# Optimization experiments

Hardware: AMD Instinct MI355X
Metric: run time of the kernel (lower is better)

Reference implementation:

```python
import jax, jax.numpy as jnp
import numpy as np
from jax import lax

EPS = 1e-5

def _silu(x):
    return x * jax.nn.sigmoid(x)

def _mamba_seq(x, ln_w, ln_b, in_w, conv_w, conv_b, xp_w, dt_w, dt_b, A_log, Dp, out_w):
    # x: [B, L, dim] token sequence
    di = conv_w.shape[0]          # d_inner
    ds = A_log.shape[1]           # d_state
    dtr = dt_w.shape[1]           # dt_rank
    kw = conv_w.shape[2]          # d_conv
    # LayerNorm
    mu = jnp.mean(x, axis=-1, keepdims=True)
    var = jnp.mean((x - mu) ** 2, axis=-1, keepdims=True)
    xn = (x - mu) * lax.rsqrt(var + EPS) * ln_w + ln_b
    # in_proj -> (x, z)
    xz = xn @ in_w.T                       # [B,L,2*di]
    xs, z = xz[..., :di], xz[..., di:]
    # causal depthwise conv1d over L
    xc = lax.conv_general_dilated(xs.transpose(0, 2, 1), conv_w, (1,),
                                  [(kw - 1, 0)], feature_group_count=di,
                                  dimension_numbers=('NCH', 'OIH', 'NCH'))
    xc = _silu(xc + conv_b[None, :, None]).transpose(0, 2, 1)   # [B,L,di]
    # x_proj -> dt, B, C
    dbc = xc @ xp_w.T                      # [B,L,dtr+2*ds]
    dt = jax.nn.softplus(dbc[..., :dtr] @ dt_w.T + dt_b)        # [B,L,di]
    Bm = dbc[..., dtr:dtr + ds]            # [B,L,ds]
    Cm = dbc[..., dtr + ds:]               # [B,L,ds]
    A = -jnp.exp(A_log)                    # [di,ds]
    dA = jnp.exp(dt[..., None] * A)        # [B,L,di,ds]
    dBu = (dt * xc)[..., None] * Bm[:, :, None, :]              # [B,L,di,ds]
    # selective scan: h_t = dA_t * h_{t-1} + dBu_t (parallel associative scan)
    def comb(e1, e2):
        a1, b1 = e1
        a2, b2 = e2
        return a1 * a2, a2 * b1 + b2
    _, h = lax.associative_scan(comb, (dA, dBu), axis=1)
    y = jnp.einsum('blds,bls->bld', h, Cm) + xc * Dp
    return (y * _silu(z)) @ out_w.T

def _mamba_block(x5, *p):
    # x5: [B,C,D,H,W] -> flatten spatial dims to tokens
    B, C = x5.shape[:2]
    xf = x5.reshape(B, C, -1).transpose(0, 2, 1)   # [B,L,C]
    y = _mamba_seq(xf, *p)
    return y.transpose(0, 2, 1).reshape(x5.shape)

def _conv3d(x, w, b):
    return lax.conv_general_dilated(x, w, (1, 1, 1), [(1, 1)] * 3,
                                    dimension_numbers=('NCDHW', 'OIDHW', 'NCDHW')) \
           + b[None, :, None, None, None]

def _bn3d(x, g, b):
    # BatchNorm3d in training mode: batch statistics over (B,D,H,W)
    m = jnp.mean(x, axis=(0, 2, 3, 4), keepdims=True)
    v = jnp.mean((x - m) ** 2, axis=(0, 2, 3, 4), keepdims=True)
    return (x - m) * lax.rsqrt(v + EPS) * g.reshape(1, -1, 1, 1, 1) + b.reshape(1, -1, 1, 1, 1)

def _mamba_params(key, dim, d_state=16, d_conv=4, expand=2):
    di = expand * dim
    dtr = max(1, -(-dim // 16))
    ks = jax.random.split(key, 5)
    return {
        'ln_w': jnp.ones((dim,), jnp.float32),
        'ln_b': jnp.zeros((dim,), jnp.float32),
        'in_w': jax.random.normal(ks[0], (2 * di, dim), jnp.float32) * (dim ** -0.5),
        'conv_w': jax.random.normal(ks[1], (di, 1, d_conv), jnp.float32) * 0.3,
        'conv_b': jnp.zeros((di,), jnp.float32),
        'xp_w': jax.random.normal(ks[2], (dtr + 2 * d_state, di), jnp.float32) * (di ** -0.5),
        'dt_w': jax.random.normal(ks[3], (di, dtr), jnp.float32) * (dtr ** -0.5),
        'dt_b': jnp.log(jnp.expm1(jnp.full((di,), 0.01, jnp.float32))),
        'A_log': jnp.log(jnp.tile(jnp.arange(1, d_state + 1, dtype=jnp.float32)[None, :], (di, 1))),
        'D': jnp.ones((di,), jnp.float32),
        'out_w': jax.random.normal(ks[4], (dim, di), jnp.float32) * (di ** -0.5),
    }

def setup_inputs() -> dict:
    key = jax.random.key(0)
    k = jax.random.split(key, 8)
    inp = {
        'l': jax.random.normal(k[0], (1, 16, 16, 48, 48), jnp.float32),
        's': jax.random.normal(k[1], (1, 16, 16, 48, 48), jnp.float32),
    }
    for name, p in _mamba_params(k[2], 32).items():
        inp['m1_' + name] = p
    for name, p in _mamba_params(k[3], 16).items():
        inp['m2_' + name] = p
    inp['c1_w'] = jax.random.normal(k[4], (16, 32, 3, 3, 3), jnp.float32) * ((32 * 27) ** -0.5)
    inp['c1_b'] = jnp.zeros((16,), jnp.float32)
    inp['bn1_g'] = jnp.ones((16,), jnp.float32)
    inp['bn1_b'] = jnp.zeros((16,), jnp.float32)
    inp['c2_w'] = jax.random.normal(k[5], (16, 16, 3, 3, 3), jnp.float32) * ((16 * 27) ** -0.5)
    inp['c2_b'] = jnp.zeros((16,), jnp.float32)
    inp['bn2_g'] = jnp.ones((16,), jnp.float32)
    inp['bn2_b'] = jnp.zeros((16,), jnp.float32)
    return inp

def reference(l, s,
              m1_ln_w, m1_ln_b, m1_in_w, m1_conv_w, m1_conv_b, m1_xp_w, m1_dt_w, m1_dt_b, m1_A_log, m1_D, m1_out_w,
              m2_ln_w, m2_ln_b, m2_in_w, m2_conv_w, m2_conv_b, m2_xp_w, m2_dt_w, m2_dt_b, m2_A_log, m2_D, m2_out_w,
              c1_w, c1_b, bn1_g, bn1_b, c2_w, c2_b, bn2_g, bn2_b):
    x = jnp.concatenate([l, s], axis=1)                         # [B,32,D,H,W]
    x = _mamba_block(x, m1_ln_w, m1_ln_b, m1_in_w, m1_conv_w, m1_conv_b,
                     m1_xp_w, m1_dt_w, m1_dt_b, m1_A_log, m1_D, m1_out_w) + x
    x = _bn3d(_conv3d(x, c1_w, c1_b), bn1_g, bn1_b)             # [B,16,D,H,W]
    x = _mamba_block(x, m2_ln_w, m2_ln_b, m2_in_w, m2_conv_w, m2_conv_b,
                     m2_xp_w, m2_dt_w, m2_dt_b, m2_A_log, m2_D, m2_out_w) + x
    x = _bn3d(_conv3d(x, c2_w, c2_b), bn2_g, bn2_b)
    return x
```

## Files before the change

### kernel.cpp

```cpp
#include <hip/hip_runtime.h>
#include <math.h>

#define L_TOT 36864
#define BN_EPS 1e-5f
#define PCH 45000

typedef __attribute__((ext_vector_type(8))) short bf16x8;
typedef __attribute__((ext_vector_type(4))) float f32x4;

__device__ __forceinline__ float fsigmoid(float x){ return 1.f/(1.f+__expf(-x)); }
__device__ __forceinline__ float fsoftplus(float x){
  float e = __expf(x);
  return (x>20.f)? x : __logf(1.f+e);
}
__device__ __forceinline__ unsigned short f2bf(float x){
  union { float f; unsigned u; } cv; cv.f = x;
  unsigned r = (cv.u + 0x7FFFu + ((cv.u>>16)&1u)) >> 16;
  return (unsigned short)r;
}
__host__ __device__ constexpr int off3c(int r){
  return (r>=27) ? 0 : ((r/9)-1)*2500 + (((r%9)/3)-1)*50 + ((r%3)-1);
}

__global__ void k_setup(const float* __restrict__ w1, unsigned short* __restrict__ wA1,
                        const float* __restrict__ w2, unsigned short* __restrict__ wA2,
                        float* __restrict__ stats, float* __restrict__ bfz) {
  int b = blockIdx.x, tid = threadIdx.x;
  int idx = b*256 + tid;
  if (idx < 16*PCH) bfz[idx] = 0.f;
  if (b < 4){
    int k = b*256 + tid;
    if (k < 864){
      int ic = k & 31, r = k >> 5;
      for (int m=0;m<16;m++){
        float v = (r < 27) ? w1[m*32*27 + ic*27 + r] : 0.f;
        wA1[(((k>>3)*16) + m)*8 + (k&7)] = f2bf(v);
      }
    }
  } else if (b < 6){
    int k = (b-4)*256 + tid;
    if (k < 448){
      int ic = k & 15, r = k >> 4;
      for (int m=0;m<16;m++){
        float v = (r < 27) ? w2[m*16*27 + ic*27 + r] : 0.f;
        wA2[(((k>>3)*16) + m)*8 + (k&7)] = f2bf(v);
      }
    }
  } else if (b == 6){
    if (tid < 64) stats[tid] = 0.f;
  }
}

template<int DIM, int DI, int DTR, bool DOBN>
__global__ __launch_bounds__(256) void k_front(
    const float* __restrict__ x0, const float* __restrict__ x1,
    const float* __restrict__ bstats, const float* __restrict__ bg, const float* __restrict__ bbp,
    const float* __restrict__ lnw, const float* __restrict__ lnb,
    const float* __restrict__ inw,
    const float* __restrict__ cw, const float* __restrict__ cb,
    const float* __restrict__ xpw,
    const float* __restrict__ dtw, const float* __restrict__ dtb,
    const float* __restrict__ Alog,
    float* __restrict__ xcg, float* __restrict__ zg,
    float* __restrict__ dtpg, float* __restrict__ Bg, float* __restrict__ Cg,
    float* __restrict__ aggA, float* __restrict__ aggB)
{
  constexpr int TCH  = 48;
  constexpr int ROWS = DTR + 32;
  constexpr int NSH  = 256/DI;
  constexpr int SPB  = 16/NSH;
  constexpr int O_SX  = 0;
  constexpr int O_SXS = O_SX + DIM*64;
  constexpr int O_SDT = O_SXS;
  constexpr int O_SXC = O_SXS + DI*64;
  constexpr int O_SB  = O_SXC + DI*49;
  constexpr int O_SC  = O_SB + 16*49;
  constexpr int O_DTP = O_SC + 16*49;
  constexpr int SMEM  = O_DTP + DTR*48 + 64;
  __shared__ float sm[SMEM];

  const int tid   = threadIdx.x;
  const int chunk = blockIdx.x;
  const int t0    = chunk*TCH;

  for (int idx = tid; idx < DIM*64; idx += 256){
    int c = idx >> 6, i = idx & 63;
    int t = t0 - 3 + i;
    float v = 0.f;
    if (i < 51 && t >= 0){
      if constexpr (DOBN){
        float raw = x0[c*L_TOT + t];
        float bm = bstats[2*c]*(1.f/L_TOT);
        float bv = bstats[2*c+1]*(1.f/L_TOT) - bm*bm;
        v = (raw - bm)*rsqrtf(bv+BN_EPS)*bg[c] + bbp[c];
      } else {
        v = (c < 16) ? x0[c*L_TOT + t] : x1[(c-16)*L_TOT + t];
      }
    }
    sm[O_SX + idx] = v;
  }
  __syncthreads();

  if (tid < 64){
    float s = 0.f, s2 = 0.f;
#pragma unroll
    for (int c = 0; c < DIM; c++){
      float v = sm[O_SX + c*64 + tid];
      s += v; s2 += v*v;
    }
    float m  = s*(1.f/DIM);
    float var = s2*(1.f/DIM) - m*m;
    float rs = rsqrtf(var + BN_EPS);
#pragma unroll
    for (int c = 0; c < DIM; c++){
      float v = sm[O_SX + c*64 + tid];
      sm[O_SX + c*64 + tid] = (v-m)*rs*lnw[c] + lnb[c];
    }
  }
  __syncthreads();

  {
    const int i  = tid & 63;
    const int r0 = __builtin_amdgcn_readfirstlane(tid >> 6);
    float xn[DIM];
#pragma unroll
    for (int c = 0; c < DIM; c++) xn[c] = sm[O_SX + c*64 + i];
    for (int r = r0; r < 2*DI; r += 4){
      float acc = 0.f;
#pragma unroll
      for (int c = 0; c < DIM; c++) acc += xn[c]*inw[r*DIM + c];
      if (r < DI){
        float v = (t0 == 0 && i < 3) ? 0.f : acc;
        if (i < 51) sm[O_SXS + r*64 + i] = v;
      } else {
        if (i >= 3 && i < 51) zg[(r-DI)*L_TOT + t0 + i - 3] = acc;
      }
    }
  }
  __syncthreads();

  for (int idx = tid; idx < DI*48; idx += 256){
    int d = idx / 48, j = idx - d*48;
    const float* xr = &sm[O_SXS + d*64 + j];
    float acc = cb[d] + cw[d*4+0]*xr[0] + cw[d*4+1]*xr[1]
                      + cw[d*4+2]*xr[2] + cw[d*4+3]*xr[3];
    sm[O_SXC + d*49 + j] = acc * fsigmoid(acc);
  }
  __syncthreads();

  {
    const int i  = tid & 63;
    const int r0 = __builtin_amdgcn_readfirstlane(tid >> 6);
    constexpr int NR = (ROWS + 3) / 4;
    float acc[NR];
#pragma unroll
    for (int rr = 0; rr < NR; rr++) acc[rr] = 0.f;
    for (int db = 0; db < DI; db += 16){
      float xcol[16];
#pragma unroll
      for (int k = 0; k < 16; k++) xcol[k] = sm[O_SXC + (db+k)*49 + i];
#pragma unroll
      for (int rr = 0; rr < NR; rr++){
        int r = r0 + rr*4;
        if (r < ROWS){
          float a = 0.f;
#pragma unroll
          for (int k = 0; k < 16; k++) a += xcol[k]*xpw[r*DI + db + k];
          acc[rr] += a;
        }
      }
    }
    if (i < 48){
#pragma unroll
      for (int rr = 0; rr < NR; rr++){
        int r = r0 + rr*4;
        if (r < ROWS){
          if (r < DTR)          sm[O_DTP + r*48 + i] = acc[rr];
          else if (r < DTR+16)  sm[O_SB + (r-DTR)*49 + i] = acc[rr];
          else                  sm[O_SC + (r-DTR-16)*49 + i] = acc[rr];
        }
      }
    }
  }
  __syncthreads();

  for (int idx = tid; idx < DI*48; idx += 256){
    int d = idx / 48, j = idx - d*48;
    float pre = dtb[d] + dtw[d*DTR]*sm[O_DTP + j];
    if (DTR > 1) pre += dtw[d*DTR + DTR-1]*sm[O_DTP + (DTR-1)*48 + j];
    sm[O_SDT + d*49 + j] = fsoftplus(pre);
  }
  __syncthreads();

  for (int idx = tid; idx < DI*12; idx += 256){
    int d = idx / 12, q = idx - d*12;
    float4 v = make_float4(sm[O_SXC + d*49 + q*4+0], sm[O_SXC + d*49 + q*4+1],
                           sm[O_SXC + d*49 + q*4+2], sm[O_SXC + d*49 + q*4+3]);
    *reinterpret_cast<float4*>(xcg + d*L_TOT + t0 + q*4) = v;
  }
  for (int idx = tid; idx < ROWS*48; idx += 256){
    int r = idx / 48, j = idx - r*48;
    if (r < DTR)         dtpg[r*L_TOT + t0 + j]        = sm[O_DTP + r*48 + j];
    else if (r < DTR+16) Bg[(r-DTR)*L_TOT + t0 + j]    = sm[O_SB + (r-DTR)*49 + j];
    else                 Cg[(r-DTR-16)*L_TOT + t0 + j] = sm[O_SC + (r-DTR-16)*49 + j];
  }

  {
    const int d  = tid / NSH;
    const int sh = tid - d*NSH;
    float Av[SPB], Ar[SPB], Br[SPB];
#pragma unroll
    for (int j = 0; j < SPB; j++){
      Av[j] = -__expf(Alog[d*16 + sh*SPB + j]);
      Ar[j] = 1.f; Br[j] = 0.f;
    }
    for (int t = 0; t < TCH; t++){
      float dtv = sm[O_SDT + d*49 + t];
      float bb2 = dtv * sm[O_SXC + d*49 + t];
#pragma unroll
      for (int j = 0; j < SPB; j++){
        float a = __expf(dtv*Av[j]);
        Ar[j] *= a;
        Br[j] = a*Br[j] + bb2*sm[O_SB + (sh*SPB+j)*49 + t];
      }
    }
    const int o = chunk*(DI*16) + tid*SPB;
#pragma unroll
    for (int j = 0; j < SPB; j++){ aggA[o+j] = Ar[j]; aggB[o+j] = Br[j]; }
  }
}

template<int NCH>
__global__ __launch_bounds__(1024) void k_carry(const float* __restrict__ aggA,
                        const float* __restrict__ aggB,
                        float* __restrict__ carry, int CH) {
  constexpr int SEG = NCH/16;
  int lane = threadIdx.x & 63;
  int seg  = threadIdx.x >> 6;
  int ch   = blockIdx.x*64 + lane;
  int c0   = seg*SEG;
  float a = 1.f, b = 0.f;
  for (int cb=c0; cb<c0+SEG; cb+=8){
    float av[8], bv[8];
#pragma unroll
    for (int k=0;k<8;k++){ av[k]=aggA[(cb+k)*CH+ch]; bv[k]=aggB[(cb+k)*CH+ch]; }
#pragma unroll
    for (int k=0;k<8;k++){ a = a*av[k]; b = av[k]*b + bv[k]; }
  }
  __shared__ float sa[16][64], sb[16][64];
  sa[seg][lane]=a; sb[seg][lane]=b;
  __syncthreads();
  if (seg==0){
    float pa=1.f, pb=0.f;
    for (int g=0; g<16; g++){
      float ca=sa[g][lane], cb2=sb[g][lane];
      sa[g][lane]=pa; sb[g][lane]=pb;
      float na = pa*ca;
      float nb = ca*pb + cb2;
      pa=na; pb=nb;
    }
  }
  __syncthreads();
  float h = sb[seg][lane];
  for (int cb=c0; cb<c0+SEG; cb+=8){
    float av[8], bv[8];
#pragma unroll
    for (int k=0;k<8;k++){ av[k]=aggA[(cb+k)*CH+ch]; bv[k]=aggB[(cb+k)*CH+ch]; }
#pragma unroll
    for (int k=0;k<8;k++){ carry[(cb+k)*CH+ch]=h; h = av[k]*h + bv[k]; }
  }
}

template<int DIM, int DI, int DTR, int RES>
__global__ __launch_bounds__(256) void k_back(
    const float* __restrict__ xcg, const float* __restrict__ zg,
    const float* __restrict__ dtpg, const float* __restrict__ Bg, const float* __restrict__ Cg,
    const float* __restrict__ dtw, const float* __restrict__ dtb,
    const float* __restrict__ Alog, const float* __restrict__ Dp,
    const float* __restrict__ carry,
    const float* __restrict__ ow,
    const float* __restrict__ r0src, const float* __restrict__ r1src,
    const float* __restrict__ bstats, const float* __restrict__ bg, const float* __restrict__ bbp,
    unsigned short* __restrict__ rp)
{
  constexpr int TCH = 48;
  constexpr int NSH = 256/DI;
  constexpr int SPB = 16/NSH;
  constexpr int O_SXC = 0;
  constexpr int O_SDT = O_SXC + DI*49;
  constexpr int O_SB  = O_SDT + DI*49;
  constexpr int O_SC  = O_SB + 16*49;
  constexpr int O_SY  = O_SC + 16*49;
  constexpr int O_DTP = O_SY + DI*49;
  constexpr int SMEM  = O_DTP + DTR*48 + 64;
  __shared__ float sm[SMEM];
  const int tid   = threadIdx.x;
  const int chunk = blockIdx.x;
  const int t0    = chunk*TCH;

  for (int idx = tid; idx < DI*12; idx += 256){
    int d = idx / 12, q = idx - d*12;
    float4 v = *reinterpret_cast<const float4*>(xcg + d*L_TOT + t0 + q*4);
    sm[O_SXC + d*49 + q*4+0] = v.x; sm[O_SXC + d*49 + q*4+1] = v.y;
    sm[O_SXC + d*49 + q*4+2] = v.z; sm[O_SXC + d*49 + q*4+3] = v.w;
  }
  for (int idx = tid; idx < (DTR+32)*48; idx += 256){
    int r = idx / 48, j = idx - r*48;
    if (r < DTR)         sm[O_DTP + r*48 + j]        = dtpg[r*L_TOT + t0 + j];
    else if (r < DTR+16) sm[O_SB + (r-DTR)*49 + j]   = Bg[(r-DTR)*L_TOT + t0 + j];
    else                 sm[O_SC + (r-DTR-16)*49 + j]= Cg[(r-DTR-16)*L_TOT + t0 + j];
  }
  __syncthreads();
  for (int idx = tid; idx < DI*48; idx += 256){
    int d = idx / 48, j = idx - d*48;
    float pre = dtb[d] + dtw[d*DTR]*sm[O_DTP + j];
    if (DTR > 1) pre += dtw[d*DTR + DTR-1]*sm[O_DTP + 48 + j];
    sm[O_SDT + d*49 + j] = fsoftplus(pre);
  }
  __syncthreads();

  {
    const int d  = tid / NSH;
    const int sh = tid - d*NSH;
    float Av[SPB], h[SPB];
#pragma unroll
    for (int j = 0; j < SPB; j++){
      Av[j] = -__expf(Alog[d*16 + sh*SPB + j]);
      h[j]  = carry[chunk*(DI*16) + tid*SPB + j];
    }
    const float Dv = Dp[d];
    for (int t = 0; t < TCH; t++){
      float dtv = sm[O_SDT + d*49 + t];
      float xcv = sm[O_SXC + d*49 + t];
      float bb2 = dtv*xcv;
      float p = 0.f;
#pragma unroll
      for (int j = 0; j < SPB; j++){
        float a = __expf(dtv*Av[j]);
        h[j] = a*h[j] + bb2*sm[O_SB + (sh*SPB+j)*49 + t];
        p += h[j]*sm[O_SC + (sh*SPB+j)*49 + t];
      }
#pragma unroll
      for (int o = 1; o < NSH; o <<= 1) p += __shfl_xor(p, o);
      if (sh == 0) sm[O_SY + d*49 + t] = p + xcv*Dv;
    }
  }
  __syncthreads();
  for (int idx = tid; idx < DI*12; idx += 256){
    int d = idx / 12, q = idx - d*12;
    float4 zv = *reinterpret_cast<const float4*>(zg + d*L_TOT + t0 + q*4);
    sm[O_SY + d*49 + q*4+0] *= zv.x*fsigmoid(zv.x);
    sm[O_SY + d*49 + q*4+1] *= zv.y*fsigmoid(zv.y);
    sm[O_SY + d*49 + q*4+2] *= zv.z*fsigmoid(zv.z);
    sm[O_SY + d*49 + q*4+3] *= zv.w*fsigmoid(zv.w);
  }
  __syncthreads();

  {
    const int col = tid & 63;
    const int r0w = __builtin_amdgcn_readfirstlane(tid >> 6);
    constexpr int NO = DIM/4;
    float acc[NO];
#pragma unroll
    for (int rr = 0; rr < NO; rr++) acc[rr] = 0.f;
    for (int db = 0; db < DI; db += 16){
      float ycol[16];
#pragma unroll
      for (int k = 0; k < 16; k++) ycol[k] = sm[O_SY + (db+k)*49 + col];
#pragma unroll
      for (int rr = 0; rr < NO; rr++){
        int r = r0w + rr*4;
        float a = 0.f;
#pragma unroll
        for (int k = 0; k < 16; k++) a += ycol[k]*ow[r*DI + db + k];
        acc[rr] += a;
      }
    }
    if (col < 48){
      const int t  = t0 + col;
      const int zz = chunk / 48, yy = chunk - zz*48;
      const int pb = (zz+1)*2500 + (yy+1)*50 + (col+1);
#pragma unroll
      for (int rr = 0; rr < NO; rr++){
        int i = r0w + rr*4;
        float res;
        if (RES == 0){
          res = (i < 16) ? r0src[i*L_TOT + t] : r1src[(i-16)*L_TOT + t];
        } else {
          float bm = bstats[2*i]*(1.f/L_TOT);
          float bv = bstats[2*i+1]*(1.f/L_TOT) - bm*bm;
          res = (r0src[i*L_TOT + t] - bm)*rsqrtf(bv+BN_EPS)*bg[i] + bbp[i];
        }
        rp[i*PCH + pb] = f2bf(acc[rr] + res);
      }
    }
  }
}

template<int IC>
__global__ __launch_bounds__(256) void k_conv_mfma(const unsigned short* __restrict__ bin,
                         const unsigned short* __restrict__ wA,
                         const float* __restrict__ bias, float* __restrict__ out,
                         float* __restrict__ stats) {
  constexpr int NKB = (IC==32) ? 27 : 14;
  __shared__ float sred[32];
  if (threadIdx.x < 32) sred[threadIdx.x] = 0.f;
  __syncthreads();
  const int lane = threadIdx.x & 63;
  const int n = lane & 15, quad = lane >> 4;
  const int tile = blockIdx.x*4 + (threadIdx.x >> 6);
  const int t = tile*16 + n;
  int zz = t / 2304;
  int r2 = t - zz*2304;
  int yy = r2 / 48;
  int xx = r2 - yy*48;
  int pb = (zz+1)*2500 + (yy+1)*50 + (xx+1);
  const unsigned short* bp[8];
#pragma unroll
  for (int j=0;j<8;j++){
    int e = quad*8 + j;
    int ic = (IC==32) ? e : (e & 15);
    bp[j] = bin + ic*PCH + pb;
  }
  const int rq = (IC==32) ? 0 : (quad >> 1);
  f32x4 acc = {0.f, 0.f, 0.f, 0.f};
#pragma unroll
  for (int kb=0; kb<NKB; kb++){
    bf16x8 af = *reinterpret_cast<const bf16x8*>(wA + (size_t)((kb*4+quad)*16 + n)*8);
    int off;
    if (IC==32) off = off3c(kb);
    else        off = rq ? off3c(2*kb+1) : off3c(2*kb);
    bf16x8 bf;
#pragma unroll
    for (int j=0;j<8;j++) bf[j] = (short)bp[j][off];
    acc = __builtin_amdgcn_mfma_f32_16x16x32_bf16(af, bf, acc, 0, 0, 0);
  }
  float vs[4];
#pragma unroll
  for (int reg=0; reg<4; reg++){
    int m = quad*4 + reg;
    float v = acc[reg] + bias[m];
    out[m*L_TOT + t] = v;
    vs[reg] = v;
  }
#pragma unroll
  for (int reg=0; reg<4; reg++){
    float a = vs[reg], b2 = vs[reg]*vs[reg];
#pragma unroll
    for (int o=1; o<16; o<<=1){ a += __shfl_xor(a,o); b2 += __shfl_xor(b2,o); }
    if (n == 0){
      atomicAdd(&sred[quad*4+reg], a);
      atomicAdd(&sred[16 + quad*4+reg], b2);
    }
  }
  __syncthreads();
  if (threadIdx.x < 16){
    atomicAdd(&stats[2*threadIdx.x],   sred[threadIdx.x]);
    atomicAdd(&stats[2*threadIdx.x+1], sred[16+threadIdx.x]);
  }
}

__global__ void k_bn_norm4(const float* __restrict__ raw, const float* __restrict__ stats,
                           const float* __restrict__ g, const float* __restrict__ b,
                           float* __restrict__ out) {
  int i = blockIdx.x*256 + threadIdx.x;
  int c = i / (L_TOT/4);
  int tq = i - c*(L_TOT/4);
  float m = stats[2*c]*(1.f/L_TOT);
  float v = stats[2*c+1]*(1.f/L_TOT) - m*m;
  float sc = rsqrtf(v+BN_EPS)*g[c];
  float bs = b[c] - m*sc;
  float4 x = *reinterpret_cast<const float4*>(raw + c*L_TOT + tq*4);
  float4 o = make_float4(x.x*sc+bs, x.y*sc+bs, x.z*sc+bs, x.w*sc+bs);
  *reinterpret_cast<float4*>(out + c*L_TOT + tq*4) = o;
}

extern "C" void kernel_launch(void* const* d_in, const int* in_sizes, int n_in,
                              void* d_out, int out_size, void* d_ws, size_t ws_size,
                              hipStream_t stream) {
  const float* l        = (const float*)d_in[0];
  const float* s        = (const float*)d_in[1];
  const float* m1_ln_w  = (const float*)d_in[2];
  const float* m1_ln_b  = (const float*)d_in[3];
  const float* m1_in_w  = (const float*)d_in[4];
  const float* m1_cw    = (const float*)d_in[5];
  const float* m1_cb    = (const float*)d_in[6];
  const float* m1_xp_w  = (const float*)d_in[7];
  const float* m1_dt_w  = (const float*)d_in[8];
  const float* m1_dt_b  = (const float*)d_in[9];
  const float* m1_Alog  = (const float*)d_in[10];
  const float* m1_D     = (const float*)d_in[11];
  const float* m1_out_w = (const float*)d_in[12];
  const float* m2_ln_w  = (const float*)d_in[13];
  const float* m2_ln_b  = (const float*)d_in[14];
  const float* m2_in_w  = (const float*)d_in[15];
  const float* m2_cw    = (const float*)d_in[16];
  const float* m2_cb    = (const float*)d_in[17];
  const float* m2_xp_w  = (const float*)d_in[18];
  const float* m2_dt_w  = (const float*)d_in[19];
  const float* m2_dt_b  = (const float*)d_in[20];
  const float* m2_Alog  = (const float*)d_in[21];
  const float* m2_D     = (const float*)d_in[22];
  const float* m2_out_w = (const float*)d_in[23];
  const float* c1_w     = (const float*)d_in[24];
  const float* c1_b     = (const float*)d_in[25];
  const float* bn1_g    = (const float*)d_in[26];
  const float* bn1_b    = (const float*)d_in[27];
  const float* c2_w     = (const float*)d_in[28];
  const float* c2_b     = (const float*)d_in[29];
  const float* bn2_g    = (const float*)d_in[30];
  const float* bn2_b    = (const float*)d_in[31];

  float* ws = (float*)d_ws;
  const size_t L = L_TOT;
  float* xc1      = ws;
  float* z1       = ws + 64*L;
  float* B1       = ws + 128*L;
  float* C1       = ws + 144*L;
  float* dtp1     = ws + 160*L;
  float* conv1raw = ws + 162*L;
  float* xc2      = ws + 178*L;
  float* z2       = ws + 210*L;
  float* conv2raw = ws + 242*L;
  float* aggA     = ws + 258*L;
  float* aggB     = aggA + 786432;
  float* carry    = aggB + 786432;
  float* stats1   = ws + 322*L;
  float* stats2   = stats1 + 32;
  unsigned short* bfin = (unsigned short*)(ws + 323*L);
  unsigned short* wA1  = (unsigned short*)(ws + 343*L);
  unsigned short* wA2  = wA1 + 13824;

  k_setup<<<2813,256,0,stream>>>(c1_w, wA1, c2_w, wA2, stats1, (float*)bfin);

  k_front<32,64,2,false><<<768,256,0,stream>>>(l, s, stats1, bn1_g, bn1_b,
      m1_ln_w, m1_ln_b, m1_in_w, m1_cw, m1_cb, m1_xp_w, m1_dt_w, m1_dt_b, m1_Alog,
      xc1, z1, dtp1, B1, C1, aggA, aggB);
  k_carry<768><<<16,1024,0,stream>>>(aggA, aggB, carry, 1024);
  k_back<32,64,2,0><<<768,256,0,stream>>>(xc1, z1, dtp1, B1, C1,
      m1_dt_w, m1_dt_b, m1_Alog, m1_D, carry, m1_out_w, l, s,
      stats1, bn1_g, bn1_b, bfin);
  k_conv_mfma<32><<<576,256,0,stream>>>(bfin, wA1, c1_b, conv1raw, stats1);

  k_front<16,32,1,true><<<768,256,0,stream>>>(conv1raw, conv1raw, stats1, bn1_g, bn1_b,
      m2_ln_w, m2_ln_b, m2_in_w, m2_cw, m2_cb, m2_xp_w, m2_dt_w, m2_dt_b, m2_Alog,
      xc2, z2, dtp1, B1, C1, aggA, aggB);
  k_carry<768><<<8,1024,0,stream>>>(aggA, aggB, carry, 512);
  k_back<16,32,1,1><<<768,256,0,stream>>>(xc2, z2, dtp1, B1, C1,
      m2_dt_w, m2_dt_b, m2_Alog, m2_D, carry, m2_out_w, conv1raw, conv1raw,
      stats1, bn1_g, bn1_b, bfin);
  k_conv_mfma<16><<<576,256,0,stream>>>(bfin, wA2, c2_b, conv2raw, stats2);
  k_bn_norm4<<<576,256,0,stream>>>(conv2raw, stats2, bn2_g, bn2_b, (float*)d_out);
}
```

Baseline: 314.2 us.

## Fuse Mamba front, carry and back kernels into one persistent kernel with grid barriers

Merges the three per-block Mamba kernels (chunk scan, carry propagation, output) into a single kernel that uses two software grid barriers. Intermediates such as xc, z, dt, B and C stay in shared memory and registers instead of going through global memory, and two launches per block are removed. The grid of 768 blocks must all be resident at once; launch_bounds(256,3) is added to help occupancy, but if not all blocks fit the barrier spins until its timeout. The carry scan now runs on only a few blocks while the rest wait at the barrier.

```diff
diff --git a/kernel.cpp b/kernel.cpp
--- a/kernel.cpp
+++ b/kernel.cpp
@@ -22,9 +22,23 @@
   return (r>=27) ? 0 : ((r/9)-1)*2500 + (((r%9)/3)-1)*50 + ((r%3)-1);
 }
 
+__device__ __forceinline__ void grid_barrier(unsigned* c, unsigned nblk){
+  __syncthreads();
+  if (threadIdx.x == 0){
+    __hip_atomic_fetch_add(c, 1u, __ATOMIC_ACQ_REL, __HIP_MEMORY_SCOPE_AGENT);
+    unsigned spins = 0;
+    while (__hip_atomic_load(c, __ATOMIC_ACQUIRE, __HIP_MEMORY_SCOPE_AGENT) < nblk){
+      __builtin_amdgcn_s_sleep(8);
+      if (++spins > (1u<<26)) break;
+    }
+  }
+  __syncthreads();
+}
+
 __global__ void k_setup(const float* __restrict__ w1, unsigned short* __restrict__ wA1,
                         const float* __restrict__ w2, unsigned short* __restrict__ wA2,
-                        float* __restrict__ stats, float* __restrict__ bfz) {
+                        float* __restrict__ stats, unsigned* __restrict__ bar,
+                        float* __restrict__ bfz) {
   int b = blockIdx.x, tid = threadIdx.x;
   int idx = b*256 + tid;
   if (idx < 16*PCH) bfz[idx] = 0.f;
@@ -48,35 +62,37 @@
     }
   } else if (b == 6){
     if (tid < 64) stats[tid] = 0.f;
-  }
-}
-
-template<int DIM, int DI, int DTR, bool DOBN>
-__global__ __launch_bounds__(256) void k_front(
-    const float* __restrict__ x0, const float* __restrict__ x1,
-    const float* __restrict__ bstats, const float* __restrict__ bg, const float* __restrict__ bbp,
-    const float* __restrict__ lnw, const float* __restrict__ lnb,
-    const float* __restrict__ inw,
-    const float* __restrict__ cw, const float* __restrict__ cb,
-    const float* __restrict__ xpw,
-    const float* __restrict__ dtw, const float* __restrict__ dtb,
-    const float* __restrict__ Alog,
-    float* __restrict__ xcg, float* __restrict__ zg,
-    float* __restrict__ dtpg, float* __restrict__ Bg, float* __restrict__ Cg,
-    float* __restrict__ aggA, float* __restrict__ aggB)
+    if (tid >= 64 && tid < 68) bar[tid-64] = 0u;
+  }
+}
+
+struct MambaArgs {
+  const float *x0, *x1, *bstats, *bg, *bbp;
+  const float *lnw, *lnb, *inw, *cw, *cb, *xpw, *dtw, *dtb, *Alog, *Dp, *ow;
+  const float *r0src, *r1src;
+  float *aggA, *aggB, *carry;
+  unsigned *bar0, *bar1;
+  unsigned short* rp;
+};
+
+template<int DIM, int DI, int DTR, bool DOBN, int RES>
+__global__ __launch_bounds__(256,3) void k_mamba(MambaArgs a)
 {
   constexpr int TCH  = 48;
+  constexpr int NCHUNK = 768;
   constexpr int ROWS = DTR + 32;
   constexpr int NSH  = 256/DI;
   constexpr int SPB  = 16/NSH;
-  constexpr int O_SX  = 0;
-  constexpr int O_SXS = O_SX + DIM*64;
-  constexpr int O_SDT = O_SXS;
-  constexpr int O_SXC = O_SXS + DI*64;
+  constexpr int CH   = DI*16;
+  constexpr int NCB  = CH/64;
+  constexpr int NZ   = DI/4;
+  constexpr int R0SZ = DI*64;
+  constexpr int O_SXC = R0SZ;
   constexpr int O_SB  = O_SXC + DI*49;
   constexpr int O_SC  = O_SB + 16*49;
-  constexpr int O_DTP = O_SC + 16*49;
-  constexpr int SMEM  = O_DTP + DTR*48 + 64;
+  constexpr int O_SY  = O_SC + 16*49;
+  constexpr int O_DTP = O_SY + DI*49;
+  constexpr int SMEM  = O_DTP + DTR*48 + 16;
   __shared__ float sm[SMEM];
 
   const int tid   = threadIdx.x;
@@ -84,20 +100,20 @@
   const int t0    = chunk*TCH;
 
   for (int idx = tid; idx < DIM*64; idx += 256){
-    int c = idx >> 6, i = idx & 63;
-    int t = t0 - 3 + i;
+    int c = idx >> 6, i2 = idx & 63;
+    int t = t0 - 3 + i2;
     float v = 0.f;
-    if (i < 51 && t >= 0){
+    if (i2 < 51 && t >= 0){
       if constexpr (DOBN){
-        float raw = x0[c*L_TOT + t];
-        float bm = bstats[2*c]*(1.f/L_TOT);
-        float bv = bstats[2*c+1]*(1.f/L_TOT) - bm*bm;
-        v = (raw - bm)*rsqrtf(bv+BN_EPS)*bg[c] + bbp[c];
+        float raw = a.x0[c*L_TOT + t];
+        float bm = a.bstats[2*c]*(1.f/L_TOT);
+        float bv = a.bstats[2*c+1]*(1.f/L_TOT) - bm*bm;
+        v = (raw - bm)*rsqrtf(bv+BN_EPS)*a.bg[c] + a.bbp[c];
       } else {
-        v = (c < 16) ? x0[c*L_TOT + t] : x1[(c-16)*L_TOT + t];
-      }
-    }
-    sm[O_SX + idx] = v;
+        v = (c < 16) ? a.x0[c*L_TOT + t] : a.x1[(c-16)*L_TOT + t];
+      }
+    }
+    sm[idx] = v;
   }
   __syncthreads();
 
@@ -105,7 +121,7 @@
     float s = 0.f, s2 = 0.f;
 #pragma unroll
     for (int c = 0; c < DIM; c++){
-      float v = sm[O_SX + c*64 + tid];
+      float v = sm[c*64 + tid];
       s += v; s2 += v*v;
     }
     float m  = s*(1.f/DIM);
@@ -113,27 +129,29 @@
     float rs = rsqrtf(var + BN_EPS);
 #pragma unroll
     for (int c = 0; c < DIM; c++){
-      float v = sm[O_SX + c*64 + tid];
-      sm[O_SX + c*64 + tid] = (v-m)*rs*lnw[c] + lnb[c];
-    }
-  }
-  __syncthreads();
-
+      float v = sm[c*64 + tid];
+      sm[c*64 + tid] = (v-m)*rs*a.lnw[c] + a.lnb[c];
+    }
+  }
+  __syncthreads();
+
+  const int i   = tid & 63;
+  const int r0w = tid >> 6;
+  float zreg[NZ];
   {
-    const int i  = tid & 63;
-    const int r0 = __builtin_amdgcn_readfirstlane(tid >> 6);
     float xn[DIM];
 #pragma unroll
-    for (int c = 0; c < DIM; c++) xn[c] = sm[O_SX + c*64 + i];
-    for (int r = r0; r < 2*DI; r += 4){
+    for (int c = 0; c < DIM; c++) xn[c] = sm[c*64 + i];
+    __syncthreads();
+    int zi = 0;
+    for (int r = r0w; r < 2*DI; r += 4){
       float acc = 0.f;
 #pragma unroll
-      for (int c = 0; c < DIM; c++) acc += xn[c]*inw[r*DIM + c];
+      for (int c = 0; c < DIM; c++) acc += xn[c]*a.inw[r*DIM + c];
       if (r < DI){
-        float v = (t0 == 0 && i < 3) ? 0.f : acc;
-        if (i < 51) sm[O_SXS + r*64 + i] = v;
+        if (i < 51) sm[r*64 + i] = (t0 == 0 && i < 3) ? 0.f : acc;
       } else {
-        if (i >= 3 && i < 51) zg[(r-DI)*L_TOT + t0 + i - 3] = acc;
+        zreg[zi++] = acc;
       }
     }
   }
@@ -141,16 +159,14 @@
 
   for (int idx = tid; idx < DI*48; idx += 256){
     int d = idx / 48, j = idx - d*48;
-    const float* xr = &sm[O_SXS + d*64 + j];
-    float acc = cb[d] + cw[d*4+0]*xr[0] + cw[d*4+1]*xr[1]
-                      + cw[d*4+2]*xr[2] + cw[d*4+3]*xr[3];
+    const float* xr = &sm[d*64 + j];
+    float acc = a.cb[d] + a.cw[d*4+0]*xr[0] + a.cw[d*4+1]*xr[1]
+                        + a.cw[d*4+2]*xr[2] + a.cw[d*4+3]*xr[3];
     sm[O_SXC + d*49 + j] = acc * fsigmoid(acc);
   }
   __syncthreads();
 
   {
-    const int i  = tid & 63;
-    const int r0 = __builtin_amdgcn_readfirstlane(tid >> 6);
     constexpr int NR = (ROWS + 3) / 4;
     float acc[NR];
 #pragma unroll
@@ -161,19 +177,19 @@
       for (int k = 0; k < 16; k++) xcol[k] = sm[O_SXC + (db+k)*49 + i];
 #pragma unroll
       for (int rr = 0; rr < NR; rr++){
-        int r = r0 + rr*4;
+        int r = r0w + rr*4;
         if (r < ROWS){
-          float a = 0.f;
-#pragma unroll
-          for (int k = 0; k < 16; k++) a += xcol[k]*xpw[r*DI + db + k];
-          acc[rr] += a;
+          float a2 = 0.f;
+#pragma unroll
+          for (int k = 0; k < 16; k++) a2 += xcol[k]*a.xpw[r*DI + db + k];
+          acc[rr] += a2;
         }
       }
     }
     if (i < 48){
 #pragma unroll
       for (int rr = 0; rr < NR; rr++){
-        int r = r0 + rr*4;
+        int r = r0w + rr*4;
         if (r < ROWS){
           if (r < DTR)          sm[O_DTP + r*48 + i] = acc[rr];
           else if (r < DTR+16)  sm[O_SB + (r-DTR)*49 + i] = acc[rr];
@@ -186,179 +202,120 @@
 
   for (int idx = tid; idx < DI*48; idx += 256){
     int d = idx / 48, j = idx - d*48;
-    float pre = dtb[d] + dtw[d*DTR]*sm[O_DTP + j];
-    if (DTR > 1) pre += dtw[d*DTR + DTR-1]*sm[O_DTP + (DTR-1)*48 + j];
-    sm[O_SDT + d*49 + j] = fsoftplus(pre);
-  }
-  __syncthreads();
-
-  for (int idx = tid; idx < DI*12; idx += 256){
-    int d = idx / 12, q = idx - d*12;
-    float4 v = make_float4(sm[O_SXC + d*49 + q*4+0], sm[O_SXC + d*49 + q*4+1],
-                           sm[O_SXC + d*49 + q*4+2], sm[O_SXC + d*49 + q*4+3]);
-    *reinterpret_cast<float4*>(xcg + d*L_TOT + t0 + q*4) = v;
-  }
-  for (int idx = tid; idx < ROWS*48; idx += 256){
-    int r = idx / 48, j = idx - r*48;
-    if (r < DTR)         dtpg[r*L_TOT + t0 + j]        = sm[O_DTP + r*48 + j];
-    else if (r < DTR+16) Bg[(r-DTR)*L_TOT + t0 + j]    = sm[O_SB + (r-DTR)*49 + j];
-    else                 Cg[(r-DTR-16)*L_TOT + t0 + j] = sm[O_SC + (r-DTR-16)*49 + j];
-  }
-
+    float pre = a.dtb[d] + a.dtw[d*DTR]*sm[O_DTP + j];
+    if (DTR > 1) pre += a.dtw[d*DTR + DTR-1]*sm[O_DTP + (DTR-1)*48 + j];
+    sm[d*49 + j] = fsoftplus(pre);
+  }
+  __syncthreads();
+
+  const int dd = tid / NSH;
+  const int sh = tid - dd*NSH;
+  float Av[SPB];
+#pragma unroll
+  for (int j = 0; j < SPB; j++) Av[j] = -__expf(a.Alog[dd*16 + sh*SPB + j]);
   {
-    const int d  = tid / NSH;
-    const int sh = tid - d*NSH;
-    float Av[SPB], Ar[SPB], Br[SPB];
-#pragma unroll
-    for (int j = 0; j < SPB; j++){
-      Av[j] = -__expf(Alog[d*16 + sh*SPB + j]);
-      Ar[j] = 1.f; Br[j] = 0.f;
-    }
+    float Ar[SPB], Br[SPB];
+#pragma unroll
+    for (int j = 0; j < SPB; j++){ Ar[j] = 1.f; Br[j] = 0.f; }
     for (int t = 0; t < TCH; t++){
-      float dtv = sm[O_SDT + d*49 + t];
-      float bb2 = dtv * sm[O_SXC + d*49 + t];
+      float dtv = sm[dd*49 + t];
+      float bb2 = dtv * sm[O_SXC + dd*49 + t];
 #pragma unroll
       for (int j = 0; j < SPB; j++){
-        float a = __expf(dtv*Av[j]);
-        Ar[j] *= a;
-        Br[j] = a*Br[j] + bb2*sm[O_SB + (sh*SPB+j)*49 + t];
-      }
-    }
-    const int o = chunk*(DI*16) + tid*SPB;
-#pragma unroll
-    for (int j = 0; j < SPB; j++){ aggA[o+j] = Ar[j]; aggB[o+j] = Br[j]; }
-  }
-}
-
-template<int NCH>
-__global__ __launch_bounds__(1024) void k_carry(const float* __restrict__ aggA,
-                        const float* __restrict__ aggB,
-                        float* __restrict__ carry, int CH) {
-  constexpr int SEG = NCH/16;
-  int lane = threadIdx.x & 63;
-  int seg  = threadIdx.x >> 6;
-  int ch   = blockIdx.x*64 + lane;
-  int c0   = seg*SEG;
-  float a = 1.f, b = 0.f;
-  for (int cb=c0; cb<c0+SEG; cb+=8){
-    float av[8], bv[8];
-#pragma unroll
-    for (int k=0;k<8;k++){ av[k]=aggA[(cb+k)*CH+ch]; bv[k]=aggB[(cb+k)*CH+ch]; }
-#pragma unroll
-    for (int k=0;k<8;k++){ a = a*av[k]; b = av[k]*b + bv[k]; }
-  }
-  __shared__ float sa[16][64], sb[16][64];
-  sa[seg][lane]=a; sb[seg][lane]=b;
-  __syncthreads();
-  if (seg==0){
-    float pa=1.f, pb=0.f;
-    for (int g=0; g<16; g++){
-      float ca=sa[g][lane], cb2=sb[g][lane];
-      sa[g][lane]=pa; sb[g][lane]=pb;
-      float na = pa*ca;
-      float nb = ca*pb + cb2;
-      pa=na; pb=nb;
-    }
-  }
-  __syncthreads();
-  float h = sb[seg][lane];
-  for (int cb=c0; cb<c0+SEG; cb+=8){
-    float av[8], bv[8];
-#pragma unroll
-    for (int k=0;k<8;k++){ av[k]=aggA[(cb+k)*CH+ch]; bv[k]=aggB[(cb+k)*CH+ch]; }
-#pragma unroll
-    for (int k=0;k<8;k++){ carry[(cb+k)*CH+ch]=h; h = av[k]*h + bv[k]; }
-  }
-}
-
-template<int DIM, int DI, int DTR, int RES>
-__global__ __launch_bounds__(256) void k_back(
-    const float* __restrict__ xcg, const float* __restrict__ zg,
-    const float* __restrict__ dtpg, const float* __restrict__ Bg, const float* __restrict__ Cg,
-    const float* __restrict__ dtw, const float* __restrict__ dtb,
-    const float* __restrict__ Alog, const float* __restrict__ Dp,
-    const float* __restrict__ carry,
-    const float* __restrict__ ow,
-    const float* __restrict__ r0src, const float* __restrict__ r1src,
-    const float* __restrict__ bstats, const float* __restrict__ bg, const float* __restrict__ bbp,
-    unsigned short* __restrict__ rp)
-{
-  constexpr int TCH = 48;
-  constexpr int NSH = 256/DI;
-  constexpr int SPB = 16/NSH;
-  constexpr int O_SXC = 0;
-  constexpr int O_SDT = O_SXC + DI*49;
-  constexpr int O_SB  = O_SDT + DI*49;
-  constexpr int O_SC  = O_SB + 16*49;
-  constexpr int O_SY  = O_SC + 16*49;
-  constexpr int O_DTP = O_SY + DI*49;
-  constexpr int SMEM  = O_DTP + DTR*48 + 64;
-  __shared__ float sm[SMEM];
-  const int tid   = threadIdx.x;
-  const int chunk = blockIdx.x;
-  const int t0    = chunk*TCH;
-
-  for (int idx = tid; idx < DI*12; idx += 256){
-    int d = idx / 12, q = idx - d*12;
-    float4 v = *reinterpret_cast<const float4*>(xcg + d*L_TOT + t0 + q*4);
-    sm[O_SXC + d*49 + q*4+0] = v.x; sm[O_SXC + d*49 + q*4+1] = v.y;
-    sm[O_SXC + d*49 + q*4+2] = v.z; sm[O_SXC + d*49 + q*4+3] = v.w;
-  }
-  for (int idx = tid; idx < (DTR+32)*48; idx += 256){
-    int r = idx / 48, j = idx - r*48;
-    if (r < DTR)         sm[O_DTP + r*48 + j]        = dtpg[r*L_TOT + t0 + j];
-    else if (r < DTR+16) sm[O_SB + (r-DTR)*49 + j]   = Bg[(r-DTR)*L_TOT + t0 + j];
-    else                 sm[O_SC + (r-DTR-16)*49 + j]= Cg[(r-DTR-16)*L_TOT + t0 + j];
-  }
-  __syncthreads();
-  for (int idx = tid; idx < DI*48; idx += 256){
-    int d = idx / 48, j = idx - d*48;
-    float pre = dtb[d] + dtw[d*DTR]*sm[O_DTP + j];
-    if (DTR > 1) pre += dtw[d*DTR + DTR-1]*sm[O_DTP + 48 + j];
-    sm[O_SDT + d*49 + j] = fsoftplus(pre);
-  }
-  __syncthreads();
+        float a2 = __expf(dtv*Av[j]);
+        Ar[j] *= a2;
+        Br[j] = a2*Br[j] + bb2*sm[O_SB + (sh*SPB+j)*49 + t];
+      }
+    }
+    const int o = chunk*CH + tid*SPB;
+    if constexpr (SPB == 4){
+      *reinterpret_cast<float4*>(&a.aggA[o]) = make_float4(Ar[0],Ar[1],Ar[2],Ar[3]);
+      *reinterpret_cast<float4*>(&a.aggB[o]) = make_float4(Br[0],Br[1],Br[2],Br[3]);
+    } else {
+      *reinterpret_cast<float2*>(&a.aggA[o]) = make_float2(Ar[0],Ar[1]);
+      *reinterpret_cast<float2*>(&a.aggB[o]) = make_float2(Br[0],Br[1]);
+    }
+  }
+  grid_barrier(a.bar0, NCHUNK);
+
+  if (blockIdx.x < NCB){
+    const int lane = tid & 63, seg = tid >> 6;
+    const int ch = blockIdx.x*64 + lane;
+    constexpr int SEG = NCHUNK/4;
+    const int c0 = seg*SEG;
+    float aa = 1.f, bb3 = 0.f;
+    for (int cb = c0; cb < c0+SEG; cb += 8){
+      float av[8], bv[8];
+#pragma unroll
+      for (int k=0;k<8;k++){ av[k]=a.aggA[(cb+k)*CH+ch]; bv[k]=a.aggB[(cb+k)*CH+ch]; }
+#pragma unroll
+      for (int k=0;k<8;k++){ aa = aa*av[k]; bb3 = av[k]*bb3 + bv[k]; }
+    }
+    float* sca = &sm[O_SY];
+    float* scb = &sm[O_SY + 256];
+    sca[seg*64+lane] = aa; scb[seg*64+lane] = bb3;
+    __syncthreads();
+    if (seg == 0){
+      float pa = 1.f, pb = 0.f;
+      for (int g = 0; g < 4; g++){
+        float ca = sca[g*64+lane], cb2 = scb[g*64+lane];
+        sca[g*64+lane] = pa; scb[g*64+lane] = pb;
+        float na = pa*ca;
+        float nb = ca*pb + cb2;
+        pa = na; pb = nb;
+      }
+    }
+    __syncthreads();
+    float h = scb[seg*64+lane];
+    for (int cb = c0; cb < c0+SEG; cb += 8){
+      float av[8], bv[8];
+#pragma unroll
+      for (int k=0;k<8;k++){ av[k]=a.aggA[(cb+k)*CH+ch]; bv[k]=a.aggB[(cb+k)*CH+ch]; }
+#pragma unroll
+      for (int k=0;k<8;k++){ a.carry[(cb+k)*CH+ch] = h; h = av[k]*h + bv[k]; }
+    }
+  }
+  grid_barrier(a.bar1, NCHUNK);
 
   {
-    const int d  = tid / NSH;
-    const int sh = tid - d*NSH;
-    float Av[SPB], h[SPB];
-#pragma unroll
-    for (int j = 0; j < SPB; j++){
-      Av[j] = -__expf(Alog[d*16 + sh*SPB + j]);
-      h[j]  = carry[chunk*(DI*16) + tid*SPB + j];
-    }
-    const float Dv = Dp[d];
+    float h[SPB];
+    const int o = chunk*CH + tid*SPB;
+    if constexpr (SPB == 4){
+      float4 hv = *reinterpret_cast<const float4*>(&a.carry[o]);
+      h[0]=hv.x; h[1]=hv.y; h[2]=hv.z; h[3]=hv.w;
+    } else {
+      float2 hv = *reinterpret_cast<const float2*>(&a.carry[o]);
+      h[0]=hv.x; h[1]=hv.y;
+    }
+    const float Dv = a.Dp[dd];
     for (int t = 0; t < TCH; t++){
-      float dtv = sm[O_SDT + d*49 + t];
-      float xcv = sm[O_SXC + d*49 + t];
+      float dtv = sm[dd*49 + t];
+      float xcv = sm[O_SXC + dd*49 + t];
       float bb2 = dtv*xcv;
       float p = 0.f;
 #pragma unroll
       for (int j = 0; j < SPB; j++){
-        float a = __expf(dtv*Av[j]);
-        h[j] = a*h[j] + bb2*sm[O_SB + (sh*SPB+j)*49 + t];
+        float a2 = __expf(dtv*Av[j]);
+        h[j] = a2*h[j] + bb2*sm[O_SB + (sh*SPB+j)*49 + t];
         p += h[j]*sm[O_SC + (sh*SPB+j)*49 + t];
       }
 #pragma unroll
-      for (int o = 1; o < NSH; o <<= 1) p += __shfl_xor(p, o);
-      if (sh == 0) sm[O_SY + d*49 + t] = p + xcv*Dv;
-    }
-  }
-  __syncthreads();
-  for (int idx = tid; idx < DI*12; idx += 256){
-    int d = idx / 12, q = idx - d*12;
-    float4 zv = *reinterpret_cast<const float4*>(zg + d*L_TOT + t0 + q*4);
-    sm[O_SY + d*49 + q*4+0] *= zv.x*fsigmoid(zv.x);
-    sm[O_SY + d*49 + q*4+1] *= zv.y*fsigmoid(zv.y);
-    sm[O_SY + d*49 + q*4+2] *= zv.z*fsigmoid(zv.z);
-    sm[O_SY + d*49 + q*4+3] *= zv.w*fsigmoid(zv.w);
+      for (int o2 = 1; o2 < NSH; o2 <<= 1) p += __shfl_xor(p, o2);
+      if (sh == 0) sm[O_SY + dd*49 + t] = p + xcv*Dv;
+    }
+  }
+  __syncthreads();
+
+  if (i >= 3 && i < 51){
+#pragma unroll
+    for (int u = 0; u < NZ; u++){
+      float zv = zreg[u];
+      sm[O_SY + (r0w + 4*u)*49 + (i-3)] *= zv*fsigmoid(zv);
+    }
   }
   __syncthreads();
 
   {
-    const int col = tid & 63;
-    const int r0w = __builtin_amdgcn_readfirstlane(tid >> 6);
     constexpr int NO = DIM/4;
     float acc[NO];
 #pragma unroll
@@ -366,32 +323,32 @@
     for (int db = 0; db < DI; db += 16){
       float ycol[16];
 #pragma unroll
-      for (int k = 0; k < 16; k++) ycol[k] = sm[O_SY + (db+k)*49 + col];
+      for (int k = 0; k < 16; k++) ycol[k] = sm[O_SY + (db+k)*49 + i];
 #pragma unroll
       for (int rr = 0; rr < NO; rr++){
         int r = r0w + rr*4;
-        float a = 0.f;
-#pragma unroll
-        for (int k = 0; k < 16; k++) a += ycol[k]*ow[r*DI + db + k];
-        acc[rr] += a;
-      }
-    }
-    if (col < 48){
-      const int t  = t0 + col;
+        float a2 = 0.f;
+#pragma unroll
+        for (int k = 0; k < 16; k++) a2 += ycol[k]*a.ow[r*DI + db + k];
+        acc[rr] += a2;
+      }
+    }
+    if (i < 48){
+      const int t  = t0 + i;
       const int zz = chunk / 48, yy = chunk - zz*48;
-      const int pb = (zz+1)*2500 + (yy+1)*50 + (col+1);
+      const int pb2 = (zz+1)*2500 + (yy+1)*50 + (i+1);
 #pragma unroll
       for (int rr = 0; rr < NO; rr++){
-        int i = r0w + rr*4;
+        int r = r0w + rr*4;
         float res;
         if (RES == 0){
-          res = (i < 16) ? r0src[i*L_TOT + t] : r1src[(i-16)*L_TOT + t];
+          res = (r < 16) ? a.r0src[r*L_TOT + t] : a.r1src[(r-16)*L_TOT + t];
         } else {
-          float bm = bstats[2*i]*(1.f/L_TOT);
-          float bv = bstats[2*i+1]*(1.f/L_TOT) - bm*bm;
-          res = (r0src[i*L_TOT + t] - bm)*rsqrtf(bv+BN_EPS)*bg[i] + bbp[i];
+          float bm = a.bstats[2*r]*(1.f/L_TOT);
+          float bv = a.bstats[2*r+1]*(1.f/L_TOT) - bm*bm;
+          res = (a.r0src[r*L_TOT + t] - bm)*rsqrtf(bv+BN_EPS)*a.bg[r] + a.bbp[r];
         }
-        rp[i*PCH + pb] = f2bf(acc[rr] + res);
+        a.rp[r*PCH + pb2] = f2bf(acc[rr] + res);
       }
     }
   }
@@ -513,42 +470,32 @@
 
   float* ws = (float*)d_ws;
   const size_t L = L_TOT;
-  float* xc1      = ws;
-  float* z1       = ws + 64*L;
-  float* B1       = ws + 128*L;
-  float* C1       = ws + 144*L;
-  float* dtp1     = ws + 160*L;
-  float* conv1raw = ws + 162*L;
-  float* xc2      = ws + 178*L;
-  float* z2       = ws + 210*L;
-  float* conv2raw = ws + 242*L;
-  float* aggA     = ws + 258*L;
+  float* conv1raw = ws;
+  float* conv2raw = ws + 16*L;
+  float* aggA     = ws + 32*L;
   float* aggB     = aggA + 786432;
   float* carry    = aggB + 786432;
-  float* stats1   = ws + 322*L;
+  float* stats1   = carry + 786432;
   float* stats2   = stats1 + 32;
-  unsigned short* bfin = (unsigned short*)(ws + 323*L);
-  unsigned short* wA1  = (unsigned short*)(ws + 343*L);
+  unsigned* bar   = (unsigned*)(stats2 + 32);
+  unsigned short* bfin = (unsigned short*)(stats2 + 48);
+  unsigned short* wA1  = bfin + 32*PCH;
   unsigned short* wA2  = wA1 + 13824;
 
-  k_setup<<<2813,256,0,stream>>>(c1_w, wA1, c2_w, wA2, stats1, (float*)bfin);
-
-  k_front<32,64,2,false><<<768,256,0,stream>>>(l, s, stats1, bn1_g, bn1_b,
-      m1_ln_w, m1_ln_b, m1_in_w, m1_cw, m1_cb, m1_xp_w, m1_dt_w, m1_dt_b, m1_Alog,
-      xc1, z1, dtp1, B1, C1, aggA, aggB);
-  k_carry<768><<<16,1024,0,stream>>>(aggA, aggB, carry, 1024);
-  k_back<32,64,2,0><<<768,256,0,stream>>>(xc1, z1, dtp1, B1, C1,
-      m1_dt_w, m1_dt_b, m1_Alog, m1_D, carry, m1_out_w, l, s,
-      stats1, bn1_g, bn1_b, bfin);
+  k_setup<<<2813,256,0,stream>>>(c1_w, wA1, c2_w, wA2, stats1, bar, (float*)bfin);
+
+  MambaArgs a1 = { l, s, stats1, bn1_g, bn1_b,
+                   m1_ln_w, m1_ln_b, m1_in_w, m1_cw, m1_cb, m1_xp_w,
+                   m1_dt_w, m1_dt_b, m1_Alog, m1_D, m1_out_w,
+                   l, s, aggA, aggB, carry, bar+0, bar+1, bfin };
+  k_mamba<32,64,2,false,0><<<768,256,0,stream>>>(a1);
   k_conv_mfma<32><<<576,256,0,stream>>>(bfin, wA1, c1_b, conv1raw, stats1);
 
-  k_front<16,32,1,true><<<768,256,0,stream>>>(conv1raw, conv1raw, stats1, bn1_g, bn1_b,
-      m2_ln_w, m2_ln_b, m2_in_w, m2_cw, m2_cb, m2_xp_w, m2_dt_w, m2_dt_b, m2_Alog,
-      xc2, z2, dtp1, B1, C1, aggA, aggB);
-  k_carry<768><<<8,1024,0,stream>>>(aggA, aggB, carry, 512);
-  k_back<16,32,1,1><<<768,256,0,stream>>>(xc2, z2, dtp1, B1, C1,
-      m2_dt_w, m2_dt_b, m2_Alog, m2_D, carry, m2_out_w, conv1raw, conv1raw,
-      stats1, bn1_g, bn1_b, bfin);
+  MambaArgs a2 = { conv1raw, conv1raw, stats1, bn1_g, bn1_b,
+                   m2_ln_w, m2_ln_b, m2_in_w, m2_cw, m2_cb, m2_xp_w,
+                   m2_dt_w, m2_dt_b, m2_Alog, m2_D, m2_out_w,
+                   conv1raw, conv1raw, aggA, aggB, carry, bar+2, bar+3, bfin };
+  k_mamba<16,32,1,true,1><<<768,256,0,stream>>>(a2);
   k_conv_mfma<16><<<576,256,0,stream>>>(bfin, wA2, c2_b, conv2raw, stats2);
   k_bn_norm4<<<576,256,0,stream>>>(conv2raw, stats2, bn2_g, bn2_b, (float*)d_out);
 }
```

After: 897.2 us. 186% more time.
